# Optimization experiments

Measured on AMD Instinct MI355X. Metric: run time of the kernel, lower is better.

## Reference

```python
import jax, jax.numpy as jnp
import numpy as np

N_NODES = 50000
N_EDGES = 400000
F_IN = 128
HID = 64
HEADS = 8
N_CLASSES = 16
NEG_SLOPE = 0.2  # PyG GATConv default negative_slope


def _glorot(key, shape):
    fan_in, fan_out = shape[0], shape[-1]
    lim = jnp.sqrt(6.0 / (fan_in + fan_out))
    return jax.random.uniform(key, shape, jnp.float32, -lim, lim)


def setup_inputs() -> dict:
    key = jax.random.key(0)
    ks = jax.random.split(key, 16)
    x = jax.random.normal(ks[0], (N_NODES, F_IN), jnp.float32)
    edge_index = jax.random.randint(ks[1], (2, N_EDGES), 0, N_NODES, jnp.int64)
    # layer 0: F_IN -> HEADS*HID (concat)
    W0 = _glorot(ks[2], (F_IN, HEADS * HID))
    a_s0 = _glorot(ks[3], (HEADS, HID))
    a_d0 = _glorot(ks[4], (HEADS, HID))
    b0 = jnp.zeros((HEADS * HID,), jnp.float32)
    # layer 1: HEADS*HID -> HEADS*HID (concat)
    W1 = _glorot(ks[5], (HEADS * HID, HEADS * HID))
    a_s1 = _glorot(ks[6], (HEADS, HID))
    a_d1 = _glorot(ks[7], (HEADS, HID))
    b1 = jnp.zeros((HEADS * HID,), jnp.float32)
    # final layer: HEADS*HID -> N_CLASSES, heads=1, concat=False (mean over heads)
    W2 = _glorot(ks[8], (HEADS * HID, 1 * N_CLASSES))
    a_s2 = _glorot(ks[9], (1, N_CLASSES))
    a_d2 = _glorot(ks[10], (1, N_CLASSES))
    b2 = jnp.zeros((N_CLASSES,), jnp.float32)
    return {"x": x, "edge_index": edge_index,
            "W0": W0, "a_s0": a_s0, "a_d0": a_d0, "b0": b0,
            "W1": W1, "a_s1": a_s1, "a_d1": a_d1, "b1": b1,
            "W2": W2, "a_s2": a_s2, "a_d2": a_d2, "b2": b2}


def gat_conv(x, src, dst, W, a_src, a_dst, b, num_nodes, concat):
    """One PyG-style GATConv (self-loops already in src/dst).
    x: [N, F_in]; W: [F_in, H*C]; a_src/a_dst: [H, C]; b: [H*C] or [C]."""
    H, C = a_src.shape
    h = (x @ W).reshape(num_nodes, H, C)                    # [N,H,C]
    al_s = jnp.einsum('nhc,hc->nh', h, a_src)               # [N,H]
    al_d = jnp.einsum('nhc,hc->nh', h, a_dst)               # [N,H]
    e = jax.nn.leaky_relu(al_s[src] + al_d[dst], NEG_SLOPE) # [E,H]
    # scatter-softmax over incoming edges of each destination node
    m = jax.ops.segment_max(e, dst, num_segments=num_nodes)  # [N,H]
    ex = jnp.exp(e - m[dst])
    denom = jax.ops.segment_sum(ex, dst, num_segments=num_nodes)
    alpha = ex / denom[dst]                                  # [E,H]
    out = jax.ops.segment_sum(alpha[:, :, None] * h[src], dst,
                              num_segments=num_nodes)        # [N,H,C]
    if concat:
        return out.reshape(num_nodes, H * C) + b
    return out.mean(axis=1) + b


def reference(x, edge_index, W0, a_s0, a_d0, b0, W1, a_s1, a_d1, b1,
              W2, a_s2, a_d2, b2):
    N = x.shape[0]
    # PyG GATConv adds self-loops by default
    loops = jnp.arange(N, dtype=edge_index.dtype)
    src = jnp.concatenate([edge_index[0], loops])
    dst = jnp.concatenate([edge_index[1], loops])
    h = gat_conv(x, src, dst, W0, a_s0, a_d0, b0, N, concat=True)
    h = jax.nn.elu(h)  # dropout is identity in eval mode
    h = gat_conv(h, src, dst, W1, a_s1, a_d1, b1, N, concat=True)
    h = jax.nn.elu(h)
    return gat_conv(h, src, dst, W2, a_s2, a_d2, b2, N, concat=False)
```

## Files before the change

kernel.cpp:

```cpp
#include <hip/hip_runtime.h>

#define N_NODES 50000
#define N_EDGES 400000
#define E_TOT   450000
#define NEG 0.2f
#define NB_SCAN ((N_NODES + 255) / 256)
#define MAXD 64

typedef unsigned short ushort_t;
typedef __attribute__((ext_vector_type(8))) _Float16 half8;
typedef __attribute__((ext_vector_type(4))) float  f32x4;
typedef __attribute__((ext_vector_type(8))) unsigned short ushort8;

__device__ __forceinline__ ushort_t f2h(float f){
    _Float16 h = (_Float16)f;
    union { _Float16 h; ushort_t u; } v; v.h = h; return v.u;
}
__device__ __forceinline__ float h_lo(unsigned u){
    union { unsigned u; _Float16 h[2]; } v; v.u = u; return (float)v.h[0];
}
__device__ __forceinline__ float h_hi(unsigned u){
    union { unsigned u; _Float16 h[2]; } v; v.u = u; return (float)v.h[1];
}
__device__ __forceinline__ void gload_lds16(const void* g, void* l){
    __builtin_amdgcn_global_load_lds((const __attribute__((address_space(1))) void*)g,
                                     (__attribute__((address_space(3))) void*)l, 16, 0, 0);
}
__device__ __forceinline__ int wave_incl_scan(int v, int lane){
    #pragma unroll
    for(int off = 1; off < 64; off <<= 1){
        int t = __shfl_up(v, off, 64);
        if(lane >= off) v += t;
    }
    return v;
}


__global__ void count_deg(const int* __restrict__ ei, int* __restrict__ deg){
    int e = blockIdx.x*256 + threadIdx.x;
    if(e >= E_TOT) return;
    int dst = (e < N_EDGES) ? ei[N_EDGES + e] : (e - N_EDGES);
    atomicAdd(&deg[dst], 1);
}

__global__ void deg_block_sum(const int* __restrict__ deg, int* __restrict__ bsum){
    int i = blockIdx.x*256 + threadIdx.x;
    int lane = threadIdx.x & 63, wave = threadIdx.x >> 6;
    int v = (i < N_NODES) ? deg[i] : 0;
    #pragma unroll
    for(int off = 1; off < 64; off <<= 1) v += __shfl_xor(v, off, 64);
    __shared__ int sw[4];
    if(lane == 0) sw[wave] = v;
    __syncthreads();
    if(threadIdx.x == 0) bsum[blockIdx.x] = sw[0] + sw[1] + sw[2] + sw[3];
}

__global__ void scan_apply(const int* __restrict__ bsum,
                           int* __restrict__ dw, int* __restrict__ rowptr){
    __shared__ int soff;
    __shared__ int sw[4];
    int i = blockIdx.x*256 + threadIdx.x;
    int lane = threadIdx.x & 63, wave = threadIdx.x >> 6;
    if(wave == 0){
        int s = 0;
        for(int j = lane; j < (int)blockIdx.x; j += 64) s += bsum[j];
        #pragma unroll
        for(int off = 1; off < 64; off <<= 1) s += __shfl_xor(s, off, 64);
        if(lane == 0) soff = s;
    }
    int v = (i < N_NODES) ? dw[i] : 0;
    int incl = wave_incl_scan(v, lane);
    if(lane == 63) sw[wave] = incl;
    __syncthreads();
    int add = soff;
    for(int w = 0; w < wave; w++) add += sw[w];
    int excl = incl - v + add;
    if(i < N_NODES){ rowptr[i] = excl; dw[i] = excl; }
    if(i == N_NODES-1) rowptr[N_NODES] = excl + v;
}

__global__ void scatter_edges(const int* __restrict__ ei, int* __restrict__ wofs,
                              int* __restrict__ csr){
    int e = blockIdx.x*256 + threadIdx.x;
    if(e >= E_TOT) return;
    int src, dst;
    if(e < N_EDGES){ src = ei[e]; dst = ei[N_EDGES + e]; }
    else { src = dst = e - N_EDGES; }
    int pos = atomicAdd(&wofs[dst], 1);
    csr[pos] = src;
}


__global__ void cvt_all(const float* __restrict__ x, const float* __restrict__ W0,
                        const float* __restrict__ W1,
                        ushort_t* __restrict__ xbf, ushort_t* __restrict__ W0t,
                        ushort_t* __restrict__ W1t, int* __restrict__ wofs){
    int i = blockIdx.x*256 + threadIdx.x;
    if(i < N_NODES*128) xbf[i] = f2h(x[i]);
    if(i < 512*128){ int n = i >> 7, k = i & 127; W0t[i] = f2h(W0[(size_t)k*512 + n]); }
    if(i < 512*512){ int n = i >> 9, k = i & 511; W1t[i] = f2h(W1[(size_t)k*512 + n]); }
    if(i < N_NODES) wofs[i] = 0;
}


template<int K>
__global__ __launch_bounds__(256) void gemm_bt(const ushort_t* __restrict__ A,
                                               const ushort_t* __restrict__ Bt,
                                               ushort_t* __restrict__ Cb,
                                               const float* __restrict__ a_s,
                                               const float* __restrict__ a_d,
                                               float* __restrict__ als,
                                               float* __restrict__ ald, int M){
    __shared__ ushort_t As[128*32];
    __shared__ ushort_t Bs[128*32];
    int tid  = threadIdx.x;
    int wave = tid >> 6, lane = tid & 63;
    int wm = wave & 1, wn = wave >> 1;
    int row0 = blockIdx.y * 128;
    int col0 = blockIdx.x * 128;

    f32x4 acc[4][4] = {};

    int lrow = lane >> 2;
    int lchk = (lane & 3) * 8;

    for(int kt = 0; kt < K; kt += 32){
        #pragma unroll
        for(int s = 0; s < 2; s++){
            int seg = wave*2 + s;
            int ar = row0 + seg*16 + lrow;
            ar = ar < M ? ar : M-1;
            gload_lds16(A  + (size_t)ar*K + kt + lchk, As + seg*512);
            int br = col0 + seg*16 + lrow;
            gload_lds16(Bt + (size_t)br*K + kt + lchk, Bs + seg*512);
        }
        __syncthreads();

        half8 a[4], b[4];
        int fm = lane & 15, fq = (lane >> 4) * 8;
        #pragma unroll
        for(int t = 0; t < 4; t++){
            a[t] = *(const half8*)&As[(wm*64 + t*16 + fm)*32 + fq];
            b[t] = *(const half8*)&Bs[(wn*64 + t*16 + fm)*32 + fq];
        }
        #pragma unroll
        for(int i = 0; i < 4; i++)
            #pragma unroll
            for(int j = 0; j < 4; j++)
                acc[i][j] = __builtin_amdgcn_mfma_f32_16x16x32_f16(a[i], b[j], acc[i][j], 0, 0, 0);
        __syncthreads();
    }

    int cm = (lane >> 4) * 4, cn = lane & 15;
    int head = (col0 + wn*64) >> 6;
    float as_[4], ad_[4];
    #pragma unroll
    for(int j = 0; j < 4; j++){
        int c = head*64 + cn + j*16;
        as_[j] = a_s[c]; ad_[j] = a_d[c];
    }
    #pragma unroll
    for(int i = 0; i < 4; i++){
        #pragma unroll
        for(int p = 0; p < 4; p++){
            int r = row0 + wm*64 + i*16 + cm + p;
            float ps = 0.f, pd = 0.f;
            if(r < M){
                ushort_t* cp = &Cb[(size_t)r*512 + col0 + wn*64 + cn];
                #pragma unroll
                for(int j = 0; j < 4; j++){
                    float v = acc[i][j][p];
                    cp[j*16] = f2h(v);
                    ps += v*as_[j]; pd += v*ad_[j];
                }
            }
            #pragma unroll
            for(int off = 1; off < 16; off <<= 1){
                ps += __shfl_xor(ps, off);
                pd += __shfl_xor(pd, off);
            }
            if(cn == 0 && r < M){ als[r*8 + head] = ps; ald[r*8 + head] = pd; }
        }
    }
}


__global__ __launch_bounds__(256) void attn_agg(const ushort_t* __restrict__ h,
        const float* __restrict__ als, const float* __restrict__ ald,
        const int* __restrict__ rowptr, const int* __restrict__ csr,
        const float* __restrict__ bias, ushort_t* __restrict__ out){
    __shared__ float sm[4][8], sd[4][8];
    __shared__ float sex[4][MAXD][8];
    int wv = threadIdx.x >> 6, lane = threadIdx.x & 63;
    int n = blockIdx.x*4 + wv;
    int start = rowptr[n], end = rowptr[n+1];

    int hd = lane & 7, e8 = lane >> 3;
    float aldv = ald[n*8 + hd];
    float lmax = -1e30f;
    for(int idx = start + e8; idx < end; idx += 8){
        int e = idx - start;
        int src = csr[idx];
        float v = als[src*8 + hd] + aldv;
        v = v > 0.f ? v : NEG*v;
        if(e < MAXD) sex[wv][e][hd] = v;
        lmax = fmaxf(lmax, v);
    }
    for(int off = 8; off < 64; off <<= 1) lmax = fmaxf(lmax, __shfl_xor(lmax, off));
    float lsum = 0.f;
    for(int idx = start + e8; idx < end; idx += 8){
        int e = idx - start;
        float v;
        if(e < MAXD) v = sex[wv][e][hd];
        else { int src = csr[idx]; v = als[src*8 + hd] + aldv; v = v > 0.f ? v : NEG*v; }
        float ex = __expf(v - lmax);
        if(e < MAXD) sex[wv][e][hd] = ex;
        lsum += ex;
    }
    for(int off = 8; off < 64; off <<= 1) lsum += __shfl_xor(lsum, off);
    if(lane < 8){ sm[wv][hd] = lmax; sd[wv][hd] = 1.f / lsum; }
    __syncthreads();

    int head = lane >> 3;
    float inv = sd[wv][head];
    float acc[8] = {};

    int cnt = end - start;
    int nmain = cnt < MAXD ? cnt : MAXD;
    int mend = start + nmain;
    int last = mend - 1;
    for(int idx = start; idx < mend; idx += 8){
        int ss[8]; uint4 pp[8]; float ee[8];
        #pragma unroll
        for(int k = 0; k < 8; k++){
            int j = idx + k;
            ss[k] = csr[j <= last ? j : last];
        }
        #pragma unroll
        for(int k = 0; k < 8; k++)
            pp[k] = *(const uint4*)&h[(size_t)ss[k]*512 + lane*8];
        #pragma unroll
        for(int k = 0; k < 8; k++){
            int j = idx + k;
            ee[k] = (j < mend) ? sex[wv][j-start][head] : 0.f;
        }
        #pragma unroll
        for(int k = 0; k < 8; k++){
            acc[0] += ee[k]*h_lo(pp[k].x); acc[1] += ee[k]*h_hi(pp[k].x);
            acc[2] += ee[k]*h_lo(pp[k].y); acc[3] += ee[k]*h_hi(pp[k].y);
            acc[4] += ee[k]*h_lo(pp[k].z); acc[5] += ee[k]*h_hi(pp[k].z);
            acc[6] += ee[k]*h_lo(pp[k].w); acc[7] += ee[k]*h_hi(pp[k].w);
        }
    }
    if(mend < end){
        float m = sm[wv][head];
        float aldn = ald[n*8 + head];
        for(int idx = mend; idx < end; idx++){
            int src = csr[idx];
            float v = als[src*8 + head] + aldn;
            v = v > 0.f ? v : NEG*v;
            float e0 = __expf(v - m);
            uint4 p = *(const uint4*)&h[(size_t)src*512 + lane*8];
            acc[0] += e0*h_lo(p.x); acc[1] += e0*h_hi(p.x);
            acc[2] += e0*h_lo(p.y); acc[3] += e0*h_hi(p.y);
            acc[4] += e0*h_lo(p.z); acc[5] += e0*h_hi(p.z);
            acc[6] += e0*h_lo(p.w); acc[7] += e0*h_hi(p.w);
        }
    }

    ushort8 o;
    #pragma unroll
    for(int j = 0; j < 8; j++){
        float v = acc[j]*inv + bias[lane*8 + j];
        v = v > 0.f ? v : (__expf(v) - 1.f);
        o[j] = f2h(v);
    }
    *(ushort8*)&out[(size_t)n*512 + lane*8] = o;
}


__global__ __launch_bounds__(256) void gemm2_k(const ushort_t* __restrict__ A,
                                               const float* __restrict__ W,
                                               const float* __restrict__ a_s2,
                                               const float* __restrict__ a_d2,
                                               float* __restrict__ C,
                                               float* __restrict__ als,
                                               float* __restrict__ ald){
    __shared__ float Ws[16][513];
    for(int i = threadIdx.x; i < 512*16; i += 256){
        int k = i >> 4, c = i & 15;
        Ws[c][k] = W[i];
    }
    __syncthreads();
    int t = blockIdx.x*256 + threadIdx.x;
    int c = t & 15;
    long row = t >> 4;
    const ushort_t* ap = &A[row*512];
    const float* wp = &Ws[c][0];
    float acc = 0.f;
    for(int k = 0; k < 512; k += 8){
        uint4 p = *(const uint4*)&ap[k];
        acc += h_lo(p.x)*wp[k+0] + h_hi(p.x)*wp[k+1]
             + h_lo(p.y)*wp[k+2] + h_hi(p.y)*wp[k+3]
             + h_lo(p.z)*wp[k+4] + h_hi(p.z)*wp[k+5]
             + h_lo(p.w)*wp[k+6] + h_hi(p.w)*wp[k+7];
    }
    C[t] = acc;
    float ps = acc * a_s2[c], pd = acc * a_d2[c];
    #pragma unroll
    for(int off = 1; off < 16; off <<= 1){
        ps += __shfl_xor(ps, off);
        pd += __shfl_xor(pd, off);
    }
    if(c == 0){ als[row] = ps; ald[row] = pd; }
}

__global__ __launch_bounds__(256) void attn_agg2(const float* __restrict__ h2,
        const float* __restrict__ als, const float* __restrict__ ald,
        const int* __restrict__ rowptr, const int* __restrict__ csr,
        const float* __restrict__ b2, float* __restrict__ out){
    int wv = threadIdx.x >> 6, lane = threadIdx.x & 63;
    int q = lane >> 4, c = lane & 15;
    int n = blockIdx.x*16 + wv*4 + q;
    int start = rowptr[n], end = rowptr[n+1];
    float aldv = ald[n];

    float lmax = -1e30f;
    for(int idx = start + c; idx < end; idx += 16){
        float v = als[csr[idx]] + aldv; v = v > 0.f ? v : NEG*v;
        lmax = fmaxf(lmax, v);
    }
    #pragma unroll
    for(int off = 1; off < 16; off <<= 1) lmax = fmaxf(lmax, __shfl_xor(lmax, off));
    float lsum = 0.f;
    for(int idx = start + c; idx < end; idx += 16){
        float v = als[csr[idx]] + aldv; v = v > 0.f ? v : NEG*v;
        lsum += __expf(v - lmax);
    }
    #pragma unroll
    for(int off = 1; off < 16; off <<= 1) lsum += __shfl_xor(lsum, off);
    float inv = 1.f / lsum;

    float acc = 0.f;
    for(int idx = start; idx < end; idx++){
        int src = csr[idx];
        float v = als[src] + aldv; v = v > 0.f ? v : NEG*v;
        float alpha = __expf(v - lmax) * inv;
        acc += alpha * h2[src*16 + c];
    }
    out[n*16 + c] = acc + b2[c];
}


extern "C" void kernel_launch(void* const* d_in, const int* in_sizes, int n_in,
                              void* d_out, int out_size, void* d_ws, size_t ws_size,
                              hipStream_t stream) {
    const float* x    = (const float*)d_in[0];
    const int*   ei   = (const int*)  d_in[1];
    const float* W0   = (const float*)d_in[2];
    const float* a_s0 = (const float*)d_in[3];
    const float* a_d0 = (const float*)d_in[4];
    const float* b0   = (const float*)d_in[5];
    const float* W1   = (const float*)d_in[6];
    const float* a_s1 = (const float*)d_in[7];
    const float* a_d1 = (const float*)d_in[8];
    const float* b1   = (const float*)d_in[9];
    const float* W2   = (const float*)d_in[10];
    const float* a_s2 = (const float*)d_in[11];
    const float* a_d2 = (const float*)d_in[12];
    const float* b2   = (const float*)d_in[13];
    float* out = (float*)d_out;

    char* w = (char*)d_ws;
    auto alloc = [&](size_t bytes){ void* p = (void*)w; w += (bytes + 255) & ~(size_t)255; return p; };
    int*      rowptr = (int*)     alloc((N_NODES+1)*sizeof(int));
    int*      wofs   = (int*)     alloc(N_NODES*sizeof(int));
    int*      bsum   = (int*)     alloc(NB_SCAN*sizeof(int));
    int*      csr    = (int*)     alloc(E_TOT*sizeof(int));
    float*    als    = (float*)   alloc((size_t)N_NODES*8*sizeof(float));
    float*    ald    = (float*)   alloc((size_t)N_NODES*8*sizeof(float));
    ushort_t* hb     = (ushort_t*)alloc((size_t)N_NODES*512*sizeof(ushort_t));
    ushort_t* hbf    = (ushort_t*)alloc((size_t)N_NODES*512*sizeof(ushort_t));
    ushort_t* xbf    = (ushort_t*)alloc((size_t)N_NODES*128*sizeof(ushort_t));
    ushort_t* W0t    = (ushort_t*)alloc((size_t)512*128*sizeof(ushort_t));
    ushort_t* W1t    = (ushort_t*)alloc((size_t)512*512*sizeof(ushort_t));
    float*    h2     = (float*)   alloc((size_t)N_NODES*16*sizeof(float));

    cvt_all<<<(N_NODES*128+255)/256, 256, 0, stream>>>(x, W0, W1, xbf, W0t, W1t, wofs);

    count_deg<<<(E_TOT+255)/256, 256, 0, stream>>>(ei, wofs);
    deg_block_sum<<<NB_SCAN, 256, 0, stream>>>(wofs, bsum);
    scan_apply<<<NB_SCAN, 256, 0, stream>>>(bsum, wofs, rowptr);
    scatter_edges<<<(E_TOT+255)/256, 256, 0, stream>>>(ei, wofs, csr);

    gemm_bt<128><<<dim3(4, (N_NODES+127)/128), 256, 0, stream>>>(xbf, W0t, hb, a_s0, a_d0, als, ald, N_NODES);
    attn_agg<<<N_NODES/4, 256, 0, stream>>>(hb, als, ald, rowptr, csr, b0, hbf);

    gemm_bt<512><<<dim3(4, (N_NODES+127)/128), 256, 0, stream>>>(hbf, W1t, hb, a_s1, a_d1, als, ald, N_NODES);
    attn_agg<<<N_NODES/4, 256, 0, stream>>>(hb, als, ald, rowptr, csr, b1, hbf);

    gemm2_k<<<(N_NODES*16)/256, 256, 0, stream>>>(hbf, W2, a_s2, a_d2, h2, als, ald);
    attn_agg2<<<N_NODES/16, 256, 0, stream>>>(h2, als, ald, rowptr, csr, b2, out);
}
```

Before: 460.8 us.

## Prefetch neighbor rows in attn_agg, MFMA final GEMM, cache exps in attn_agg2

attn_agg now issues the first batch of neighbor feature loads before the softmax pass and double-buffers the next batch of 8 rows while accumulating the current one. The goal is to hide gather latency, and it is paired with a launch_bounds occupancy hint. The final 512->16 projection moves from a scalar fp32 loop to fp16 MFMA 16x16x32, using a W2 transpose produced in cvt_all. attn_agg2 caches edge scores and exponentials in shared memory so the aggregation loop no longer recomputes them. The changes raise register pressure and add fp16 rounding of W2.

```diff
diff --git a/kernel.cpp b/kernel.cpp
--- a/kernel.cpp
+++ b/kernel.cpp
@@ -92,13 +92,15 @@
 
 
 __global__ void cvt_all(const float* __restrict__ x, const float* __restrict__ W0,
-                        const float* __restrict__ W1,
+                        const float* __restrict__ W1, const float* __restrict__ W2,
                         ushort_t* __restrict__ xbf, ushort_t* __restrict__ W0t,
-                        ushort_t* __restrict__ W1t, int* __restrict__ wofs){
+                        ushort_t* __restrict__ W1t, ushort_t* __restrict__ W2t,
+                        int* __restrict__ wofs){
     int i = blockIdx.x*256 + threadIdx.x;
     if(i < N_NODES*128) xbf[i] = f2h(x[i]);
     if(i < 512*128){ int n = i >> 7, k = i & 127; W0t[i] = f2h(W0[(size_t)k*512 + n]); }
     if(i < 512*512){ int n = i >> 9, k = i & 511; W1t[i] = f2h(W1[(size_t)k*512 + n]); }
+    if(i < 16*512){ int n = i >> 9, k = i & 511; W2t[i] = f2h(W2[(size_t)k*16 + n]); }
     if(i < N_NODES) wofs[i] = 0;
 }
 
@@ -185,7 +187,7 @@
 }
 
 
-__global__ __launch_bounds__(256) void attn_agg(const ushort_t* __restrict__ h,
+__global__ __launch_bounds__(256, 4) void attn_agg(const ushort_t* __restrict__ h,
         const float* __restrict__ als, const float* __restrict__ ald,
         const int* __restrict__ rowptr, const int* __restrict__ csr,
         const float* __restrict__ bias, ushort_t* __restrict__ out){
@@ -194,6 +196,19 @@
     int wv = threadIdx.x >> 6, lane = threadIdx.x & 63;
     int n = blockIdx.x*4 + wv;
     int start = rowptr[n], end = rowptr[n+1];
+
+    int cnt = end - start;
+    int nmain = cnt < MAXD ? cnt : MAXD;
+    int mend = start + nmain;
+    int last = mend - 1;
+
+    uint4 pp[8];
+    #pragma unroll
+    for(int k = 0; k < 8; k++){
+        int j = start + k;
+        int s = csr[j <= last ? j : last];
+        pp[k] = *(const uint4*)&h[(size_t)s*512 + lane*8];
+    }
 
     int hd = lane & 7, e8 = lane >> 3;
     float aldv = ald[n*8 + hd];
@@ -225,24 +240,24 @@
     float inv = sd[wv][head];
     float acc[8] = {};
 
-    int cnt = end - start;
-    int nmain = cnt < MAXD ? cnt : MAXD;
-    int mend = start + nmain;
-    int last = mend - 1;
-    for(int idx = start; idx < mend; idx += 8){
-        int ss[8]; uint4 pp[8]; float ee[8];
-        #pragma unroll
-        for(int k = 0; k < 8; k++){
-            int j = idx + k;
-            ss[k] = csr[j <= last ? j : last];
-        }
-        #pragma unroll
-        for(int k = 0; k < 8; k++)
-            pp[k] = *(const uint4*)&h[(size_t)ss[k]*512 + lane*8];
+    int idx = start;
+    for(;;){
+        float ee[8];
         #pragma unroll
         for(int k = 0; k < 8; k++){
             int j = idx + k;
             ee[k] = (j < mend) ? sex[wv][j-start][head] : 0.f;
+        }
+        int nidx = idx + 8;
+        bool more = nidx < mend;
+        uint4 np[8];
+        if(more){
+            #pragma unroll
+            for(int k = 0; k < 8; k++){
+                int j = nidx + k;
+                int s = csr[j <= last ? j : last];
+                np[k] = *(const uint4*)&h[(size_t)s*512 + lane*8];
+            }
         }
         #pragma unroll
         for(int k = 0; k < 8; k++){
@@ -251,12 +266,17 @@
             acc[4] += ee[k]*h_lo(pp[k].z); acc[5] += ee[k]*h_hi(pp[k].z);
             acc[6] += ee[k]*h_lo(pp[k].w); acc[7] += ee[k]*h_hi(pp[k].w);
         }
-    }
+        if(!more) break;
+        #pragma unroll
+        for(int k = 0; k < 8; k++) pp[k] = np[k];
+        idx = nidx;
+    }
+
     if(mend < end){
         float m = sm[wv][head];
         float aldn = ald[n*8 + head];
-        for(int idx = mend; idx < end; idx++){
-            int src = csr[idx];
+        for(int ix = mend; ix < end; ix++){
+            int src = csr[ix];
             float v = als[src*8 + head] + aldn;
             v = v > 0.f ? v : NEG*v;
             float e0 = __expf(v - m);
@@ -279,76 +299,95 @@
 }
 
 
-__global__ __launch_bounds__(256) void gemm2_k(const ushort_t* __restrict__ A,
-                                               const float* __restrict__ W,
-                                               const float* __restrict__ a_s2,
-                                               const float* __restrict__ a_d2,
-                                               float* __restrict__ C,
-                                               float* __restrict__ als,
-                                               float* __restrict__ ald){
-    __shared__ float Ws[16][513];
-    for(int i = threadIdx.x; i < 512*16; i += 256){
-        int k = i >> 4, c = i & 15;
-        Ws[c][k] = W[i];
-    }
-    __syncthreads();
-    int t = blockIdx.x*256 + threadIdx.x;
-    int c = t & 15;
-    long row = t >> 4;
-    const ushort_t* ap = &A[row*512];
-    const float* wp = &Ws[c][0];
-    float acc = 0.f;
-    for(int k = 0; k < 512; k += 8){
-        uint4 p = *(const uint4*)&ap[k];
-        acc += h_lo(p.x)*wp[k+0] + h_hi(p.x)*wp[k+1]
-             + h_lo(p.y)*wp[k+2] + h_hi(p.y)*wp[k+3]
-             + h_lo(p.z)*wp[k+4] + h_hi(p.z)*wp[k+5]
-             + h_lo(p.w)*wp[k+6] + h_hi(p.w)*wp[k+7];
-    }
-    C[t] = acc;
-    float ps = acc * a_s2[c], pd = acc * a_d2[c];
-    #pragma unroll
-    for(int off = 1; off < 16; off <<= 1){
-        ps += __shfl_xor(ps, off);
-        pd += __shfl_xor(pd, off);
-    }
-    if(c == 0){ als[row] = ps; ald[row] = pd; }
+__global__ __launch_bounds__(256) void gemm2_mfma(const ushort_t* __restrict__ A,
+                                                  const ushort_t* __restrict__ W2t,
+                                                  const float* __restrict__ a_s2,
+                                                  const float* __restrict__ a_d2,
+                                                  float* __restrict__ C,
+                                                  float* __restrict__ als,
+                                                  float* __restrict__ ald){
+    int wave = threadIdx.x >> 6, lane = threadIdx.x & 63;
+    long row0 = (long)(blockIdx.x*4 + wave)*16;
+    int fr = lane & 15, fq = lane >> 4;
+    long ar = row0 + fr;
+    if(ar > N_NODES-1) ar = N_NODES-1;
+    const ushort_t* ap = A + ar*512 + fq*8;
+    const ushort_t* bp = W2t + (size_t)fr*512 + fq*8;
+    f32x4 acc = {};
+    #pragma unroll
+    for(int kt = 0; kt < 512; kt += 32){
+        half8 a = *(const half8*)(ap + kt);
+        half8 b = *(const half8*)(bp + kt);
+        acc = __builtin_amdgcn_mfma_f32_16x16x32_f16(a, b, acc, 0, 0, 0);
+    }
+    float as_ = a_s2[fr], ad_ = a_d2[fr];
+    #pragma unroll
+    for(int p = 0; p < 4; p++){
+        long r = row0 + fq*4 + p;
+        float v = acc[p];
+        float ps = v*as_, pd = v*ad_;
+        #pragma unroll
+        for(int off = 1; off < 16; off <<= 1){
+            ps += __shfl_xor(ps, off);
+            pd += __shfl_xor(pd, off);
+        }
+        if(r < N_NODES){
+            C[r*16 + fr] = v;
+            if(fr == 0){ als[r] = ps; ald[r] = pd; }
+        }
+    }
 }
 
 __global__ __launch_bounds__(256) void attn_agg2(const float* __restrict__ h2,
         const float* __restrict__ als, const float* __restrict__ ald,
         const int* __restrict__ rowptr, const int* __restrict__ csr,
         const float* __restrict__ b2, float* __restrict__ out){
+    __shared__ float sex2[16][MAXD+1];
     int wv = threadIdx.x >> 6, lane = threadIdx.x & 63;
     int q = lane >> 4, c = lane & 15;
-    int n = blockIdx.x*16 + wv*4 + q;
+    int slot = wv*4 + q;
+    int n = blockIdx.x*16 + slot;
     int start = rowptr[n], end = rowptr[n+1];
     float aldv = ald[n];
+    int cnt = end - start;
+    int nmain = cnt < MAXD ? cnt : MAXD;
+    int mend = start + nmain;
 
     float lmax = -1e30f;
     for(int idx = start + c; idx < end; idx += 16){
+        int e = idx - start;
         float v = als[csr[idx]] + aldv; v = v > 0.f ? v : NEG*v;
+        if(e < MAXD) sex2[slot][e] = v;
         lmax = fmaxf(lmax, v);
     }
     #pragma unroll
     for(int off = 1; off < 16; off <<= 1) lmax = fmaxf(lmax, __shfl_xor(lmax, off));
     float lsum = 0.f;
     for(int idx = start + c; idx < end; idx += 16){
-        float v = als[csr[idx]] + aldv; v = v > 0.f ? v : NEG*v;
-        lsum += __expf(v - lmax);
+        int e = idx - start;
+        float v;
+        if(e < MAXD) v = sex2[slot][e];
+        else { v = als[csr[idx]] + aldv; v = v > 0.f ? v : NEG*v; }
+        float ex = __expf(v - lmax);
+        if(e < MAXD) sex2[slot][e] = ex;
+        lsum += ex;
     }
     #pragma unroll
     for(int off = 1; off < 16; off <<= 1) lsum += __shfl_xor(lsum, off);
     float inv = 1.f / lsum;
 
     float acc = 0.f;
-    for(int idx = start; idx < end; idx++){
+    for(int idx = start; idx < mend; idx++){
+        int src = csr[idx];
+        float ex = sex2[slot][idx - start];
+        acc += ex * h2[(size_t)src*16 + c];
+    }
+    for(int idx = mend; idx < end; idx++){
         int src = csr[idx];
         float v = als[src] + aldv; v = v > 0.f ? v : NEG*v;
-        float alpha = __expf(v - lmax) * inv;
-        acc += alpha * h2[src*16 + c];
-    }
-    out[n*16 + c] = acc + b2[c];
+        acc += __expf(v - lmax) * h2[(size_t)src*16 + c];
+    }
+    out[(size_t)n*16 + c] = acc*inv + b2[c];
 }
 
 
@@ -384,9 +423,10 @@
     ushort_t* xbf    = (ushort_t*)alloc((size_t)N_NODES*128*sizeof(ushort_t));
     ushort_t* W0t    = (ushort_t*)alloc((size_t)512*128*sizeof(ushort_t));
     ushort_t* W1t    = (ushort_t*)alloc((size_t)512*512*sizeof(ushort_t));
+    ushort_t* W2t    = (ushort_t*)alloc((size_t)16*512*sizeof(ushort_t));
     float*    h2     = (float*)   alloc((size_t)N_NODES*16*sizeof(float));
 
-    cvt_all<<<(N_NODES*128+255)/256, 256, 0, stream>>>(x, W0, W1, xbf, W0t, W1t, wofs);
+    cvt_all<<<(N_NODES*128+255)/256, 256, 0, stream>>>(x, W0, W1, W2, xbf, W0t, W1t, W2t, wofs);
 
     count_deg<<<(E_TOT+255)/256, 256, 0, stream>>>(ei, wofs);
     deg_block_sum<<<NB_SCAN, 256, 0, stream>>>(wofs, bsum);
@@ -399,6 +439,6 @@
     gemm_bt<512><<<dim3(4, (N_NODES+127)/128), 256, 0, stream>>>(hbf, W1t, hb, a_s1, a_d1, als, ald, N_NODES);
     attn_agg<<<N_NODES/4, 256, 0, stream>>>(hb, als, ald, rowptr, csr, b1, hbf);
 
-    gemm2_k<<<(N_NODES*16)/256, 256, 0, stream>>>(hbf, W2, a_s2, a_d2, h2, als, ald);
+    gemm2_mfma<<<(N_NODES+63)/64, 256, 0, stream>>>(hbf, W2t, a_s2, a_d2, h2, als, ald);
     attn_agg2<<<N_NODES/16, 256, 0, stream>>>(h2, als, ald, rowptr, csr, b2, out);
 }
```

After: 451.4 us. 1.02x faster.
